# Kernel optimization log

Hardware: AMD Instinct MI355X
Metric: run time of the kernel (lower is better)

## Reference

```python
import jax, jax.numpy as jnp
import numpy as np

B, S, H = 2, 1024, 4096
NH, NKV, HD = 32, 8, 128
GROUPS = NH // NKV  # 4


def _dequant_linear(x, w_q, scale, bias=None):
    # torch Linear layout: W [out, in]; per-output-channel symmetric dequant
    w = w_q.astype(jnp.float32) * scale[:, None]
    y = jnp.einsum('bsi,oi->bso', x, w)
    if bias is not None:
        y = y + bias
    return y


def setup_inputs() -> dict:
    key = jax.random.key(0)
    ks = jax.random.split(key, 12)
    hidden_states = jax.random.normal(ks[0], (B, S, H), dtype=jnp.float32)
    # additive causal mask: 0 on/below diagonal, large negative above
    causal = jnp.where(jnp.tril(jnp.ones((S, S), dtype=bool)), 0.0, -1e9).astype(jnp.float32)
    attention_mask = jnp.broadcast_to(causal[None, None], (B, 1, S, S))
    # int8-valued quantized weights, per-out-channel scales (~unit-variance effective weight rows / sqrt(fan_in))
    def qw(k, out, inp):
        return jax.random.randint(k, (out, inp), -127, 128, dtype=jnp.int32)
    def sc(k, out):
        return jax.random.uniform(k, (out,), dtype=jnp.float32, minval=1e-4, maxval=3e-4)
    wq_q = qw(ks[1], H, H);            wq_s = sc(ks[2], H)
    wk_q = qw(ks[3], NKV * HD, H);     wk_s = sc(ks[4], NKV * HD)
    wv_q = qw(ks[5], NKV * HD, H);     wv_s = sc(ks[6], NKV * HD)
    wo_q = qw(ks[7], H, H);            wo_s = sc(ks[8], H)
    bq = jax.random.normal(ks[9], (H,), dtype=jnp.float32) * 0.02
    bk = jax.random.normal(ks[10], (NKV * HD,), dtype=jnp.float32) * 0.02
    return {
        'hidden_states': hidden_states, 'attention_mask': attention_mask,
        'wq_q': wq_q, 'wq_s': wq_s, 'bq': bq,
        'wk_q': wk_q, 'wk_s': wk_s, 'bk': bk,
        'wv_q': wv_q, 'wv_s': wv_s,
        'wo_q': wo_q, 'wo_s': wo_s,
    }


def reference(hidden_states, attention_mask, wq_q, wq_s, bq, wk_q, wk_s, bk, wv_q, wv_s, wo_q, wo_s):
    bsz, q_len, _ = hidden_states.shape
    q = _dequant_linear(hidden_states, wq_q, wq_s, bq)      # [B,S,H]
    k = _dequant_linear(hidden_states, wk_q, wk_s, bk)      # [B,S,NKV*HD]
    v = _dequant_linear(hidden_states, wv_q, wv_s)          # [B,S,NKV*HD]
    q = q.reshape(bsz, q_len, NH, HD).transpose(0, 2, 1, 3)     # [B,NH,S,HD]
    k = k.reshape(bsz, q_len, NKV, HD).transpose(0, 2, 1, 3)    # [B,NKV,S,HD]
    v = v.reshape(bsz, q_len, NKV, HD).transpose(0, 2, 1, 3)
    # GQA: repeat_interleave kv heads along head dim
    k = jnp.repeat(k, GROUPS, axis=1)   # [B,NH,S,HD]
    v = jnp.repeat(v, GROUPS, axis=1)
    scores = jnp.einsum('bhqd,bhkd->bhqk', q, k) / np.float32(np.sqrt(HD))
    scores = scores + attention_mask
    attn = jax.nn.softmax(scores.astype(jnp.float32), axis=-1).astype(q.dtype)
    out = jnp.einsum('bhqk,bhkd->bhqd', attn, v)            # [B,NH,S,HD]
    out = out.transpose(0, 2, 1, 3).reshape(bsz, q_len, H)
    out = _dequant_linear(out, wo_q, wo_s)
    return out
```

## Files before the change

kernel.cpp:

```cpp
#include <hip/hip_runtime.h>
#include <math.h>

#define BB   2
#define SS   1024
#define HH   4096
#define NHH  32
#define NKVV 8
#define HDD  128
#define MR   2048
#define KVD  1024
#define NQKVD 6144
#define KD   4096
#define SCALE2_F 0.12751744f

typedef __attribute__((ext_vector_type(8))) short bf16x8;
typedef __attribute__((ext_vector_type(4))) float f32x4;
typedef __attribute__((ext_vector_type(4))) int i32x4;

#define MFMA(a, b, c) __builtin_amdgcn_mfma_f32_16x16x32_bf16((a), (b), (c), 0, 0, 0)
#define MFMA_I8(a, b, c) __builtin_amdgcn_mfma_i32_16x16x64_i8((a), (b), (c), 0, 0, 0)

__device__ __forceinline__ unsigned short f2bf(float f) {
  union { float f; unsigned u; } v; v.f = f;
  return (unsigned short)((v.u + 0x7fffu + ((v.u >> 16) & 1u)) >> 16);
}
__device__ __forceinline__ float bf2f(unsigned short s) {
  union { unsigned u; float f; } v; v.u = ((unsigned)s) << 16; return v.f;
}
__device__ __forceinline__ float exp2_fast(float x) {
  float r; asm("v_exp_f32 %0, %1" : "=v"(r) : "v"(x)); return r;
}
__device__ __forceinline__ unsigned cvt_pk_bf16(float a, float b) {
  unsigned r; asm("v_cvt_pk_bf16_f32 %0, %1, %2" : "=v"(r) : "v"(a), "v"(b)); return r;
}

__device__ __forceinline__ void gload_lds16(const void* g, void* l) {
  __builtin_amdgcn_global_load_lds(
      (const __attribute__((address_space(1))) void*)g,
      (__attribute__((address_space(3))) void*)l, 16, 0, 0);
}

__device__ __forceinline__ signed char q8(float x, float inv) {
  float r = rintf(x * inv);
  r = fmaxf(-127.f, fminf(127.f, r));
  return (signed char)(int)r;
}

#define NQ16 ((size_t)HH * HH / 16)
#define NK16 ((size_t)KVD * HH / 16)
__global__ void cvt_w_all(const int* __restrict__ wq, const int* __restrict__ wk,
                          const int* __restrict__ wv, const int* __restrict__ wo,
                          signed char* __restrict__ wqkv, signed char* __restrict__ wo8) {
  size_t i = (size_t)blockIdx.x * 256 + threadIdx.x;
  const int* src;
  signed char* dst;
  if (i < NQ16) { src = wq; dst = wqkv; }
  else if (i < NQ16 + NK16) { src = wk - NQ16 * 16; dst = wqkv; }
  else if (i < NQ16 + 2 * NK16) { src = wv - (NQ16 + NK16) * 16; dst = wqkv; }
  else { src = wo - (NQ16 + 2 * NK16) * 16; dst = wo8 - (NQ16 + 2 * NK16) * 16; }
  const int4* p = (const int4*)(src + i * 16);
  union { signed char c[16]; int4 q; } o;
#pragma unroll
  for (int j = 0; j < 4; ++j) {
    int4 v = p[j];
    o.c[j * 4 + 0] = (signed char)v.x; o.c[j * 4 + 1] = (signed char)v.y;
    o.c[j * 4 + 2] = (signed char)v.z; o.c[j * 4 + 3] = (signed char)v.w;
  }
  *(int4*)(dst + i * 16) = o.q;
}

__global__ void quant_f32(const float* __restrict__ in, signed char* __restrict__ out,
                          float* __restrict__ scale) {
  __shared__ float wm[4];
  const int row = blockIdx.x;
  const int t = threadIdx.x;
  const float4* p = (const float4*)(in + (size_t)row * HH) + t * 4;
  float4 v[4];
  float m = 0.f;
#pragma unroll
  for (int j = 0; j < 4; ++j) {
    v[j] = p[j];
    m = fmaxf(m, fmaxf(fmaxf(fabsf(v[j].x), fabsf(v[j].y)), fmaxf(fabsf(v[j].z), fabsf(v[j].w))));
  }
#pragma unroll
  for (int o = 32; o; o >>= 1) m = fmaxf(m, __shfl_xor(m, o));
  if ((t & 63) == 0) wm[t >> 6] = m;
  __syncthreads();
  m = fmaxf(fmaxf(wm[0], wm[1]), fmaxf(wm[2], wm[3]));
  m = fmaxf(m, 1e-12f);
  const float inv = 127.f / m;
  union { signed char c[16]; int4 q; } o;
#pragma unroll
  for (int j = 0; j < 4; ++j) {
    o.c[j * 4 + 0] = q8(v[j].x, inv); o.c[j * 4 + 1] = q8(v[j].y, inv);
    o.c[j * 4 + 2] = q8(v[j].z, inv); o.c[j * 4 + 3] = q8(v[j].w, inv);
  }
  ((int4*)(out + (size_t)row * HH))[t] = o.q;
  if (t == 0) scale[row] = m / 127.f;
}

__global__ void quant_bf16(const unsigned short* __restrict__ in, signed char* __restrict__ out,
                           float* __restrict__ scale) {
  __shared__ float wm[4];
  const int row = blockIdx.x;
  const int t = threadIdx.x;
  const uint4* p = (const uint4*)(in + (size_t)row * HH) + t * 2;
  float f[16];
  float m = 0.f;
#pragma unroll
  for (int j = 0; j < 2; ++j) {
    uint4 d = p[j];
    unsigned u[4] = {d.x, d.y, d.z, d.w};
#pragma unroll
    for (int k = 0; k < 4; ++k) {
      f[j * 8 + k * 2] = bf2f((unsigned short)(u[k] & 0xffff));
      f[j * 8 + k * 2 + 1] = bf2f((unsigned short)(u[k] >> 16));
    }
  }
#pragma unroll
  for (int e = 0; e < 16; ++e) m = fmaxf(m, fabsf(f[e]));
#pragma unroll
  for (int o = 32; o; o >>= 1) m = fmaxf(m, __shfl_xor(m, o));
  if ((t & 63) == 0) wm[t >> 6] = m;
  __syncthreads();
  m = fmaxf(fmaxf(wm[0], wm[1]), fmaxf(wm[2], wm[3]));
  m = fmaxf(m, 1e-12f);
  const float inv = 127.f / m;
  union { signed char c[16]; int4 q; } o;
#pragma unroll
  for (int e = 0; e < 16; ++e) o.c[e] = q8(f[e], inv);
  ((int4*)(out + (size_t)row * HH))[t] = o.q;
  if (t == 0) scale[row] = m / 127.f;
}

template <int MODE>
__global__ __launch_bounds__(256) void gemm_i8(
    const signed char* __restrict__ A, const signed char* __restrict__ W,
    const float* __restrict__ sRow,
    const float* __restrict__ s0, const float* __restrict__ s1, const float* __restrict__ s2,
    const float* __restrict__ bQ, const float* __restrict__ bK,
    unsigned short* __restrict__ oQ, unsigned short* __restrict__ oK,
    unsigned short* __restrict__ oVt, float* __restrict__ oF) {
  __shared__ signed char ldsA[128 * 128];
  __shared__ signed char ldsB[128 * 128];
  const int t = threadIdx.x;
  const int lane = t & 63;
  const int w = t >> 6;
  const int wr = w & 1, wc = w >> 1;
  const int l15 = lane & 15, quad = lane >> 4;
  const int bm = blockIdx.y, bn = blockIdx.x;

  const int srow_ = t >> 3;
  const int scol_ = ((t & 7) ^ (srow_ & 7)) * 16;
  const signed char* gA = A + (size_t)(bm * 128 + srow_) * KD + scol_;
  const signed char* gW = W + (size_t)(bn * 128 + srow_) * KD + scol_;
  signed char* lA = ldsA + t * 16;
  signed char* lB = ldsB + t * 16;

  i32x4 acc[4][4] = {};

  for (int k0 = 0; k0 < KD; k0 += 128) {
    __syncthreads();
#pragma unroll
    for (int j = 0; j < 4; ++j) {
      gload_lds16(gA + (size_t)j * 32 * KD + k0, lA + j * 4096);
      gload_lds16(gW + (size_t)j * 32 * KD + k0, lB + j * 4096);
    }
    __syncthreads();
#pragma unroll
    for (int kc = 0; kc < 2; ++kc) {
      i32x4 af[4], bfr[4];
#pragma unroll
      for (int mi = 0; mi < 4; ++mi) {
        const int row = wr * 64 + mi * 16 + l15;
        const int ch = (kc * 4 + quad) ^ (row & 7);
        af[mi] = *(const i32x4*)(ldsA + row * 128 + ch * 16);
      }
#pragma unroll
      for (int ni = 0; ni < 4; ++ni) {
        const int row = wc * 64 + ni * 16 + l15;
        const int ch = (kc * 4 + quad) ^ (row & 7);
        bfr[ni] = *(const i32x4*)(ldsB + row * 128 + ch * 16);
      }
#pragma unroll
      for (int mi = 0; mi < 4; ++mi)
#pragma unroll
        for (int ni = 0; ni < 4; ++ni)
          acc[mi][ni] = MFMA_I8(af[mi], bfr[ni], acc[mi][ni]);
    }
  }

  const int row0 = bm * 128 + wr * 64 + quad * 4;
  const int col0 = bn * 128 + wc * 64 + l15;
  if (MODE == 1) {
#pragma unroll
    for (int ni = 0; ni < 4; ++ni) {
      const int col = col0 + ni * 16;
      const float sc = s0[col];
#pragma unroll
      for (int mi = 0; mi < 4; ++mi)
#pragma unroll
        for (int r = 0; r < 4; ++r) {
          const int row = row0 + mi * 16 + r;
          oF[(size_t)row * HH + col] = (float)acc[mi][ni][r] * sRow[row] * sc;
        }
    }
  } else if (col0 < HH) {
#pragma unroll
    for (int ni = 0; ni < 4; ++ni) {
      const int col = col0 + ni * 16;
      const float sc = s0[col];
      const float bv = bQ[col];
#pragma unroll
      for (int mi = 0; mi < 4; ++mi)
#pragma unroll
        for (int r = 0; r < 4; ++r) {
          const int row = row0 + mi * 16 + r;
          oQ[(size_t)row * HH + col] =
              f2bf(((float)acc[mi][ni][r] * sRow[row] * sc + bv) * SCALE2_F);
        }
    }
  } else if (col0 < HH + KVD) {
#pragma unroll
    for (int ni = 0; ni < 4; ++ni) {
      const int col = col0 + ni * 16;
      const float sc = s1[col - HH];
      const float bv = bK[col - HH];
#pragma unroll
      for (int mi = 0; mi < 4; ++mi)
#pragma unroll
        for (int r = 0; r < 4; ++r) {
          const int row = row0 + mi * 16 + r;
          oK[(size_t)row * KVD + (col - HH)] =
              f2bf((float)acc[mi][ni][r] * sRow[row] * sc + bv);
        }
    }
  } else {
#pragma unroll
    for (int ni = 0; ni < 4; ++ni) {
      const int c = col0 + ni * 16 - (HH + KVD);
      const float sc = s2[c];
#pragma unroll
      for (int mi = 0; mi < 4; ++mi) {
        union { unsigned short s[4]; unsigned long long d; } pk;
#pragma unroll
        for (int r = 0; r < 4; ++r) {
          const int row = row0 + mi * 16 + r;
          pk.s[r] = f2bf((float)acc[mi][ni][r] * sRow[row] * sc);
        }
        *(unsigned long long*)(oVt + (size_t)c * MR + row0 + mi * 16) = pk.d;
      }
    }
  }
}

__global__ __launch_bounds__(256, 2) void attn_kernel(
    const unsigned short* __restrict__ Q,
    const unsigned short* __restrict__ K,
    const unsigned short* __restrict__ Vt,
    unsigned short* __restrict__ O) {
  __shared__ unsigned short ldsK[2][64][128];
  __shared__ unsigned short ldsV[2][2 * 128 * 32];
  __shared__ unsigned short ldsP[4][16 * 88];
  const int t = threadIdx.x;
  const int lane = t & 63;
  const int wv = t >> 6;
  const int l15 = lane & 15, quad = lane >> 4;
  const int qt = 15 - blockIdx.x;
  const int h = blockIdx.y;
  const int b = blockIdx.z;
  const int kv = h >> 2;
  const int q0w = qt * 64 + wv * 16;
  const int q = q0w + l15;

  bf16x8 bq[4];
  const unsigned short* qbase = Q + (size_t)(b * SS + q0w + l15) * HH + h * HDD + quad * 8;
#pragma unroll
  for (int kk = 0; kk < 4; ++kk) bq[kk] = *(const bf16x8*)(qbase + kk * 32);

  const int srow = t >> 4;
  const int schunk = (t & 15) ^ (srow & 7);
  const unsigned short* gK = K + (size_t)(b * SS + srow) * KVD + kv * HDD + schunk * 8;
  const unsigned short* gV = Vt + (size_t)(kv * HDD + wv * 32 + (lane >> 2)) * MR + b * SS + (lane & 3) * 8;
  unsigned short* lV = &ldsV[0][0] + wv * 1024 + lane * 8;
  unsigned short* lp = ldsP[wv];

  f32x4 accO[8] = {};
  float m_run = -1e30f, l_part = 0.f;

#pragma unroll
  for (int j = 0; j < 4; ++j)
    gload_lds16(gK + (size_t)j * 16 * KVD, &ldsK[0][j * 16][0] + t * 8);
#pragma unroll
  for (int kc = 0; kc < 2; ++kc)
#pragma unroll
    for (int j = 0; j < 2; ++j)
      gload_lds16(gV + (size_t)j * 16 * MR + kc * 32, lV + kc * 4096 + j * 512);
  __syncthreads();

  int cur = 0;
  for (int kt = 0; kt <= qt; ++kt) {
    const int k0 = kt * 64;
    if (kt < qt) {
#pragma unroll
      for (int j = 0; j < 4; ++j)
        gload_lds16(gK + (size_t)(k0 + 64 + j * 16) * KVD,
                    &ldsK[cur ^ 1][j * 16][0] + t * 8);
#pragma unroll
      for (int kc = 0; kc < 2; ++kc)
#pragma unroll
        for (int j = 0; j < 2; ++j)
          gload_lds16(gV + (size_t)j * 16 * MR + k0 + 64 + kc * 32,
                      lV + (cur ^ 1) * 8192 + kc * 4096 + j * 512);
    }

    f32x4 st[4] = {};
    __builtin_amdgcn_s_setprio(1);
#pragma unroll
    for (int kk = 0; kk < 4; ++kk)
#pragma unroll
      for (int mf = 0; mf < 4; ++mf) {
        const int r = mf * 16 + l15;
        bf16x8 af = *(const bf16x8*)(&ldsK[cur][r][((kk * 4 + quad) ^ (r & 7)) * 8]);
        st[mf] = MFMA(af, bq[kk], st[mf]);
      }
    __builtin_amdgcn_s_setprio(0);

    float p[4][4];
#pragma unroll
    for (int mf = 0; mf < 4; ++mf)
#pragma unroll
      for (int r = 0; r < 4; ++r) p[mf][r] = st[mf][r];
    if (kt == qt) {
#pragma unroll
      for (int mf = 0; mf < 4; ++mf)
#pragma unroll
        for (int r = 0; r < 4; ++r) {
          const int k = k0 + mf * 16 + quad * 4 + r;
          if (k > q) p[mf][r] = -1e30f;
        }
    }
    float cm = -1e30f;
#pragma unroll
    for (int mf = 0; mf < 4; ++mf)
#pragma unroll
      for (int r = 0; r < 4; ++r) cm = fmaxf(cm, p[mf][r]);
    cm = fmaxf(cm, __shfl_xor(cm, 16));
    cm = fmaxf(cm, __shfl_xor(cm, 32));

    if (!__all(cm <= m_run + 8.f)) {
      const float mn = fmaxf(m_run, cm);
      const float al = exp2_fast(m_run - mn);
      l_part *= al;
      m_run = mn;
      float af4[4];
#pragma unroll
      for (int r = 0; r < 4; ++r) af4[r] = __shfl(al, quad * 4 + r);
#pragma unroll
      for (int cb = 0; cb < 8; ++cb)
#pragma unroll
        for (int r = 0; r < 4; ++r) accO[cb][r] *= af4[r];
    }

#pragma unroll
    for (int mf = 0; mf < 4; ++mf) {
      const float e0 = exp2_fast(p[mf][0] - m_run);
      const float e1 = exp2_fast(p[mf][1] - m_run);
      const float e2 = exp2_fast(p[mf][2] - m_run);
      const float e3 = exp2_fast(p[mf][3] - m_run);
      l_part += (e0 + e1) + (e2 + e3);
      union { unsigned u[2]; unsigned long long d; } pk;
      pk.u[0] = cvt_pk_bf16(e0, e1);
      pk.u[1] = cvt_pk_bf16(e2, e3);
      *(unsigned long long*)(lp + l15 * 88 + mf * 16 + quad * 4) = pk.d;
    }
    bf16x8 ap0 = *(const bf16x8*)(lp + l15 * 88 + quad * 8);
    bf16x8 ap1 = *(const bf16x8*)(lp + l15 * 88 + 32 + quad * 8);

    __builtin_amdgcn_s_setprio(1);
#pragma unroll
    for (int cb = 0; cb < 8; ++cb) {
      bf16x8 bv0 = *(const bf16x8*)(&ldsV[cur][0] + (cb * 16 + l15) * 32 + quad * 8);
      bf16x8 bv1 = *(const bf16x8*)(&ldsV[cur][0] + 4096 + (cb * 16 + l15) * 32 + quad * 8);
      accO[cb] = MFMA(ap0, bv0, accO[cb]);
      accO[cb] = MFMA(ap1, bv1, accO[cb]);
    }
    __builtin_amdgcn_s_setprio(0);

    __syncthreads();
    cur ^= 1;
  }

  l_part += __shfl_xor(l_part, 16);
  l_part += __shfl_xor(l_part, 32);
  float lr[4];
#pragma unroll
  for (int r = 0; r < 4; ++r) lr[r] = __shfl(l_part, quad * 4 + r);
  unsigned short* ob = O + (size_t)(b * SS + q0w + quad * 4) * HH + h * HDD + l15;
#pragma unroll
  for (int cb = 0; cb < 8; ++cb)
#pragma unroll
    for (int r = 0; r < 4; ++r)
      ob[(size_t)r * HH + cb * 16] = f2bf(accO[cb][r] / lr[r]);
}

extern "C" void kernel_launch(void* const* d_in, const int* in_sizes, int n_in,
                              void* d_out, int out_size, void* d_ws, size_t ws_size,
                              hipStream_t stream) {
  const float* x = (const float*)d_in[0];
  const int* wq = (const int*)d_in[2];
  const float* wqs = (const float*)d_in[3];
  const float* bq = (const float*)d_in[4];
  const int* wk = (const int*)d_in[5];
  const float* wks = (const float*)d_in[6];
  const float* bk = (const float*)d_in[7];
  const int* wv = (const int*)d_in[8];
  const float* wvs = (const float*)d_in[9];
  const int* wo = (const int*)d_in[10];
  const float* wos = (const float*)d_in[11];
  float* out = (float*)d_out;
  char* ws = (char*)d_ws;

  signed char*    x_i8    = (signed char*)   (ws + (0ull   << 20));
  signed char*    wqkv_i8 = (signed char*)   (ws + (8ull   << 20));
  signed char*    wo_i8   = (signed char*)   (ws + (32ull  << 20));
  unsigned short* q_bf    = (unsigned short*)(ws + (48ull  << 20));
  unsigned short* k_bf    = (unsigned short*)(ws + (64ull  << 20));
  unsigned short* v_t     = (unsigned short*)(ws + (68ull  << 20));
  unsigned short* a_bf    = (unsigned short*)(ws + (72ull  << 20));
  signed char*    a_i8    = (signed char*)   (ws + (88ull  << 20));
  float*          sx      = (float*)         (ws + (128ull << 20));
  float*          sa      = (float*)         (ws + (129ull << 20));
  if (ws_size < (130ull << 20)) return;

  quant_f32<<<MR, 256, 0, stream>>>(x, x_i8, sx);
  cvt_w_all<<<10240, 256, 0, stream>>>(wq, wk, wv, wo, wqkv_i8, wo_i8);

  gemm_i8<0><<<dim3(NQKVD / 128, MR / 128), 256, 0, stream>>>(
      x_i8, wqkv_i8, sx, wqs, wks, wvs, bq, bk, q_bf, k_bf, v_t, nullptr);

  attn_kernel<<<dim3(16, NHH, BB), 256, 0, stream>>>(q_bf, k_bf, v_t, a_bf);

  quant_bf16<<<MR, 256, 0, stream>>>(a_bf, a_i8, sa);

  gemm_i8<1><<<dim3(HH / 128, MR / 128), 256, 0, stream>>>(
      a_i8, wo_i8, sa, wos, nullptr, nullptr, nullptr, nullptr,
      nullptr, nullptr, nullptr, out);
}
```

Baseline: 398.8 us.

## Double-buffer LDS tiles in int8 GEMM to overlap global loads with MFMA

Doubles the LDS staging buffers for the int8 GEMM and prefetches the next K tile while computing on the current one, using vmcnt waits and raw barriers instead of two __syncthreads per iteration. It aims to hide global-to-LDS load latency behind the matrix-core work. The cost is 64KB of LDS per block, which may lower occupancy, and the hand-written waitcnt/barrier ordering, which has to be exactly right to stay correct.

```diff
diff --git a/kernel.cpp b/kernel.cpp
--- a/kernel.cpp
+++ b/kernel.cpp
@@ -141,8 +141,8 @@
     const float* __restrict__ bQ, const float* __restrict__ bK,
     unsigned short* __restrict__ oQ, unsigned short* __restrict__ oK,
     unsigned short* __restrict__ oVt, float* __restrict__ oF) {
-  __shared__ signed char ldsA[128 * 128];
-  __shared__ signed char ldsB[128 * 128];
+  __shared__ signed char ldsA[2 * 128 * 128];
+  __shared__ signed char ldsB[2 * 128 * 128];
   const int t = threadIdx.x;
   const int lane = t & 63;
   const int w = t >> 6;
@@ -159,14 +159,15 @@
 
   i32x4 acc[4][4] = {};
 
-  for (int k0 = 0; k0 < KD; k0 += 128) {
-    __syncthreads();
+  auto STAGE = [&](int buf, int k0) {
+    const int bo = buf << 14;
 #pragma unroll
     for (int j = 0; j < 4; ++j) {
-      gload_lds16(gA + (size_t)j * 32 * KD + k0, lA + j * 4096);
-      gload_lds16(gW + (size_t)j * 32 * KD + k0, lB + j * 4096);
-    }
-    __syncthreads();
+      gload_lds16(gA + (size_t)j * 32 * KD + k0, lA + bo + j * 4096);
+      gload_lds16(gW + (size_t)j * 32 * KD + k0, lB + bo + j * 4096);
+    }
+  };
+  auto COMPUTE = [&](int bufo) {
 #pragma unroll
     for (int kc = 0; kc < 2; ++kc) {
       i32x4 af[4], bfr[4];
@@ -174,13 +175,13 @@
       for (int mi = 0; mi < 4; ++mi) {
         const int row = wr * 64 + mi * 16 + l15;
         const int ch = (kc * 4 + quad) ^ (row & 7);
-        af[mi] = *(const i32x4*)(ldsA + row * 128 + ch * 16);
+        af[mi] = *(const i32x4*)(ldsA + bufo + row * 128 + ch * 16);
       }
 #pragma unroll
       for (int ni = 0; ni < 4; ++ni) {
         const int row = wc * 64 + ni * 16 + l15;
         const int ch = (kc * 4 + quad) ^ (row & 7);
-        bfr[ni] = *(const i32x4*)(ldsB + row * 128 + ch * 16);
+        bfr[ni] = *(const i32x4*)(ldsB + bufo + row * 128 + ch * 16);
       }
 #pragma unroll
       for (int mi = 0; mi < 4; ++mi)
@@ -188,6 +189,25 @@
         for (int ni = 0; ni < 4; ++ni)
           acc[mi][ni] = MFMA_I8(af[mi], bfr[ni], acc[mi][ni]);
     }
+  };
+
+  STAGE(0, 0);
+#pragma unroll 1
+  for (int ti = 1; ti < KD / 128; ++ti) {
+    STAGE(ti & 1, ti * 128);
+    asm volatile("s_waitcnt vmcnt(8)" ::: "memory");
+    __builtin_amdgcn_s_barrier();
+    int bufo = ((ti & 1) ^ 1) << 14;
+    asm volatile("" : "+v"(bufo));
+    COMPUTE(bufo);
+    __builtin_amdgcn_s_barrier();
+  }
+  asm volatile("s_waitcnt vmcnt(0)" ::: "memory");
+  __builtin_amdgcn_s_barrier();
+  {
+    int bufo = ((KD / 128 - 1) & 1) << 14;
+    asm volatile("" : "+v"(bufo));
+    COMPUTE(bufo);
   }
 
   const int row0 = bm * 128 + wr * 64 + quad * 4;
```

Result: no change. 406.2 us (+1.8%).
